# Optimization experiments

Measured on AMD Instinct MI355X. Metric: run time of the kernel, lower is better.

## Reference

```python
import jax, jax.numpy as jnp
import numpy as np

K = 1048576          # number of shooting particles (k); x also has K points
LR = 0.25            # fixed-point gradient-descent learning rate
N_ITERS = 20         # nr_of_fixed_point_iterations
nl = jnp.tanh        # nonlinearity='tanh'


def _advect(z, t1, b1, t2, b2):
    # z: [n, 2, 1]; t*: [2,2]; b*: [2,1]. dot z = theta1 @ nl(theta2 @ z + b2) + b1
    return jnp.matmul(t1, nl(jnp.matmul(t2, z) + b2)) + b1


def _lagrangian(t1, b1, t2, b2, q, p, invK, invKb):
    eye = jnp.eye(2, dtype=t1.dtype)
    v1 = t1.reshape(-1)
    v2 = (t2 - eye).reshape(-1)
    kinetic = 0.5 * (v1 @ invK @ v1 + v2 @ invK @ v2
                     + b1[:, 0] @ invKb @ b1[:, 0] + b2[:, 0] @ invKb @ b2[:, 0])
    potential = jnp.mean(p * _advect(q, t1, b1, t2, b2))
    return kinetic - potential


def _run_fixed_point(q, p, t1, b1, t2, b2, invK, invKb):
    grad_fn = jax.grad(_lagrangian, argnums=(0, 1, 2, 3))
    def step(carry, _):
        t1, b1, t2, b2 = carry
        g1, gb1, g2, gb2 = grad_fn(t1, b1, t2, b2, q, p, invK, invKb)
        return (t1 - LR * g1, b1 - LR * gb1, t2 - LR * g2, b2 - LR * gb2), None
    carry, _ = jax.lax.scan(step, (t1, b1, t2, b2), None, length=N_ITERS)
    return carry


def setup_inputs() -> dict:
    key = jax.random.key(0)
    k1, k2, k3, k4, k5 = jax.random.split(key, 5)
    inp = jax.random.normal(k1, (3 * K, 1, 2), dtype=jnp.float32)
    return {
        "t": jnp.zeros((1,), dtype=jnp.float32),
        "inp": inp,
        "theta1_init": jax.random.normal(k2, (2, 2), dtype=jnp.float32),
        "bias1_init": jax.random.normal(k3, (2, 1), dtype=jnp.float32),
        "theta2_init": jax.random.normal(k4, (2, 2), dtype=jnp.float32),
        "bias2_init": jax.random.normal(k5, (2, 1), dtype=jnp.float32),
        "inv_Kbar": jnp.eye(4, dtype=jnp.float32),    # Kbar = I(d^2) -> inverse = I
        "inv_Kbar_b": jnp.eye(2, dtype=jnp.float32),  # Kbar_b = I(d) -> inverse = I
        "k": K,
    }


def reference(t, inp, theta1_init, bias1_init, theta2_init, bias2_init,
              inv_Kbar, inv_Kbar_b, k):
    qt, pt, xt = inp[:k], inp[k:2 * k], inp[2 * k:]
    q = jnp.swapaxes(qt, 1, 2)  # [k, 2, 1]
    p = jnp.swapaxes(pt, 1, 2)
    x = jnp.swapaxes(xt, 1, 2)

    def final_thetas(qv):
        return _run_fixed_point(qv, p, theta1_init, bias1_init,
                                theta2_init, bias2_init, inv_Kbar, inv_Kbar_b)

    t1, b1, t2, b2 = final_thetas(q)

    # dot_p = dL/dq of the final Lagrangian, including dependence of the
    # fixed-point thetas on q (torch uses create_graph=True throughout).
    def L_of_q(qv):
        ft1, fb1, ft2, fb2 = final_thetas(qv)
        return _lagrangian(ft1, fb1, ft2, fb2, qv, p, inv_Kbar, inv_Kbar_b)

    dot_p = jax.grad(L_of_q)(q)
    dot_x = _advect(x, t1, b1, t2, b2)
    dot_q = _advect(q, t1, b1, t2, b2)

    return jnp.concatenate([jnp.swapaxes(dot_q, 1, 2),
                            jnp.swapaxes(dot_p, 1, 2),
                            jnp.swapaxes(dot_x, 1, 2)], axis=0)
```

## Files before the change

kernel.cpp:

```cpp
#include <hip/hip_runtime.h>


#define LR 0.25f
#define NIT 20
#define RTPB 512
#define NBR 256

typedef float v2f __attribute__((ext_vector_type(2)));

__device__ __forceinline__ v2f tanh2(v2f x){
    v2f e;
    e.x = __expf(x.x + x.x);
    e.y = __expf(x.y + x.y);
    v2f d = e + 1.0f;
    v2f r;
    r.x = __builtin_amdgcn_rcpf(d.x);
    r.y = __builtin_amdgcn_rcpf(d.y);
    return 1.0f - (r + r);
}

#define DPP_ADD(x, ctrl) ((x) + __int_as_float(__builtin_amdgcn_update_dpp(0, __float_as_int(x), (ctrl), 0xF, 0xF, true)))
__device__ __forceinline__ float wave_sum64(float x){
    x = DPP_ADD(x, 0x111);
    x = DPP_ADD(x, 0x112);
    x = DPP_ADD(x, 0x114);
    x = DPP_ADD(x, 0x118);
    x = DPP_ADD(x, 0x142);
    x = DPP_ADD(x, 0x143);
    return x;
}

__device__ __forceinline__ void compute_grad(const float* s, const float* th,
                                             const float* ksym, const float* ksymb,
                                             float c, float* g){
    const float Ivec[4]={1.f,0.f,0.f,1.f};
    #pragma unroll
    for(int j=0;j<4;j++){
        float kv=0.f;
        #pragma unroll
        for(int m=0;m<4;m++) kv += ksym[j*4+m]*th[m];
        g[j] = kv - c*s[j];
    }
    #pragma unroll
    for(int i2=0;i2<2;i2++)
        g[4+i2] = ksymb[i2*2+0]*th[4] + ksymb[i2*2+1]*th[5] - c*s[4+i2];
    #pragma unroll
    for(int j=0;j<4;j++){
        float kv=0.f;
        #pragma unroll
        for(int m=0;m<4;m++) kv += ksym[j*4+m]*(th[6+m]-Ivec[m]);
        g[6+j] = kv - c*s[6+j];
    }
    #pragma unroll
    for(int i2=0;i2<2;i2++)
        g[10+i2] = ksymb[i2*2+0]*th[10] + ksymb[i2*2+1]*th[11] - c*s[10+i2];
}

template<bool FULL>
__device__ __forceinline__ void accum_sample2(v2f Q0, v2f Q1, v2f P0, v2f P1,
    float t1_00,float t1_01,float t1_10,float t1_11,
    float t2_00,float t2_01,float t2_10,float t2_11,float b2_0,float b2_1,
    v2f* acc){
    v2f u0 = t2_00*Q0 + t2_01*Q1 + b2_0;
    v2f u1 = t2_10*Q0 + t2_11*Q1 + b2_1;
    v2f h0 = tanh2(u0), h1 = tanh2(u1);
    v2f s0 = 1.0f - h0*h0, s1 = 1.0f - h1*h1;
    v2f a0 = t1_00*P0 + t1_10*P1;
    v2f a1 = t1_01*P0 + t1_11*P1;
    v2f w0 = a0*s0, w1 = a1*s1;
    acc[0]+=P0*h0; acc[1]+=P0*h1; acc[2]+=P1*h0; acc[3]+=P1*h1;
    acc[4]+=P0;    acc[5]+=P1;
    acc[6]+=w0*Q0; acc[7]+=w0*Q1; acc[8]+=w1*Q0; acc[9]+=w1*Q1;
    acc[10]+=w0;   acc[11]+=w1;
    if(FULL){
        v2f r0 = -2.0f*(a0*h0)*s0, r1 = -2.0f*(a1*h1)*s1;
        v2f ps00=P0*s0, ps01=P0*s1, ps10=P1*s0, ps11=P1*s1;
        acc[12]+=ps00*Q0; acc[13]+=ps00*Q1; acc[14]+=ps01*Q0; acc[15]+=ps01*Q1;
        acc[16]+=ps10*Q0; acc[17]+=ps10*Q1; acc[18]+=ps11*Q0; acc[19]+=ps11*Q1;
        acc[20]+=ps00; acc[21]+=ps01; acc[22]+=ps10; acc[23]+=ps11;
        v2f r0q0=r0*Q0, r1q0=r1*Q0;
        acc[24]+=r0q0*Q0; acc[25]+=r0q0*Q1; acc[26]+=r0*(Q1*Q1);
        acc[27]+=r1q0*Q0; acc[28]+=r1q0*Q1; acc[29]+=r1*(Q1*Q1);
        acc[30]+=r0q0; acc[31]+=r0*Q1; acc[32]+=r1q0; acc[33]+=r1*Q1;
        acc[34]+=r0; acc[35]+=r1;
    }
}

template<bool FULL>
__global__ __launch_bounds__(RTPB) void k_reduce(
    const float4* __restrict__ q4, const float4* __restrict__ p4, int nv4,
    const float* __restrict__ t1i, const float* __restrict__ b1i,
    const float* __restrict__ t2i, const float* __restrict__ b2i,
    const float* __restrict__ invK, const float* __restrict__ invKb,
    const float* __restrict__ theta_prev,
    const float* __restrict__ part_prev,
    float* __restrict__ part_out,
    float* __restrict__ theta_out,
    float c)
{
    constexpr int NS = FULL ? 36 : 12;
    const int tid = threadIdx.x;
    const int NT = gridDim.x*RTPB;

    __shared__ float ths[12];
    __shared__ float sgv[12];
    __shared__ float tsum[12][33];
    __shared__ float red[RTPB/64][NS];
    __shared__ float ks[16], ksb[4];

    const bool structured = (nv4 == NBR*RTPB*4);
    float4 qd[4], pd[4];
    if(structured){
        const int xcd = blockIdx.x & 7, bi = blockIdx.x >> 3;
        const int sliceSz = nv4 >> 3;
        const int base = xcd*sliceSz + bi*RTPB + tid;
        #pragma unroll
        for(int s=0;s<4;s++){ qd[s]=q4[base + s*(32*RTPB)]; pd[s]=p4[base + s*(32*RTPB)]; }
    }

    if(!part_prev){
        if(tid < 12){
            float v = (tid<4)? t1i[tid] : (tid<6)? b1i[tid-4]
                    : (tid<10)? t2i[tid-6] : b2i[tid-10];
            ths[tid] = v;
            if(blockIdx.x==0) theta_out[tid] = v;
        }
        __syncthreads();
    }else{
        if(tid < 16) ks[tid]  = 0.5f*(invK[tid]  + invK[(tid&3)*4 + (tid>>2)]);
        if(tid < 4)  ksb[tid] = 0.5f*(invKb[tid] + invKb[(tid&1)*2 + (tid>>1)]);
        if(tid < 12*32){
            int j = tid >> 5, ch = tid & 31;
            const float* col = part_prev + j*NBR;
            float s = 0.f;
            #pragma unroll
            for(int i = 0; i < NBR/32; i++) s += col[ch + i*32];
            tsum[j][ch] = s;
        }
        __syncthreads();
        if(tid < 12){
            float s = 0.f;
            #pragma unroll
            for(int ch=0; ch<32; ch++) s += tsum[tid][ch];
            sgv[tid] = s;
        }
        __syncthreads();
        if(tid == 0){
            float g[12], tp[12];
            #pragma unroll
            for(int j=0;j<12;j++) tp[j] = theta_prev[j];
            compute_grad(sgv, tp, ks, ksb, c, g);
            #pragma unroll
            for(int j=0;j<12;j++){
                float t = tp[j] - LR*g[j];
                ths[j] = t;
                if(blockIdx.x==0) theta_out[j] = t;
            }
        }
        __syncthreads();
    }

    const float t1_00=ths[0], t1_01=ths[1], t1_10=ths[2], t1_11=ths[3];
    const float t2_00=ths[6], t2_01=ths[7], t2_10=ths[8], t2_11=ths[9];
    const float b2_0=ths[10], b2_1=ths[11];

    v2f acc[NS];
    #pragma unroll
    for(int j=0;j<NS;j++) acc[j] = (v2f){0.f, 0.f};

    if(structured){
        #pragma unroll
        for(int s=0;s<4;s++){
            v2f Q0={qd[s].x,qd[s].z}, Q1={qd[s].y,qd[s].w};
            v2f P0={pd[s].x,pd[s].z}, P1={pd[s].y,pd[s].w};
            accum_sample2<FULL>(Q0,Q1,P0,P1,
                t1_00,t1_01,t1_10,t1_11,t2_00,t2_01,t2_10,t2_11,b2_0,b2_1,acc);
        }
    }else{
        for(int j = blockIdx.x*RTPB + tid; j < nv4; j += NT){
            float4 qq = q4[j], pp = p4[j];
            v2f Q0={qq.x,qq.z}, Q1={qq.y,qq.w};
            v2f P0={pp.x,pp.z}, P1={pp.y,pp.w};
            accum_sample2<FULL>(Q0,Q1,P0,P1,
                t1_00,t1_01,t1_10,t1_11,t2_00,t2_01,t2_10,t2_11,b2_0,b2_1,acc);
        }
    }

    const int wave = tid >> 6;
    float wres[NS];
    #pragma unroll
    for(int j=0;j<NS;j++) wres[j] = wave_sum64(acc[j].x + acc[j].y);
    if((tid & 63) == 63){
        #pragma unroll
        for(int j=0;j<NS;j++) red[wave][j] = wres[j];
    }
    __syncthreads();
    if(tid < NS){
        float sum = 0.f;
        #pragma unroll
        for(int w=0; w<RTPB/64; w++) sum += red[w][tid];
        part_out[tid*NBR + blockIdx.x] = sum;
    }
}

__global__ __launch_bounds__(1024) void k_backfold(
    const float* __restrict__ part,
    const float* __restrict__ thetaAll,
    const float* __restrict__ invK, const float* __restrict__ invKb,
    float* __restrict__ pk_g, float c)
{
    const int tid = threadIdx.x;
    const int wave = tid >> 6, lane = tid & 63;
    __shared__ float sums[(NIT+1)*36];
    __shared__ float ks[16], ksb[4];
    if(tid < 16) ks[tid]  = 0.5f*(invK[tid]  + invK[(tid&3)*4 + (tid>>2)]);
    if(tid < 4)  ksb[tid] = 0.5f*(invKb[tid] + invKb[(tid&1)*2 + (tid>>1)]);

    for(int seg = wave; seg < (NIT+1)*36; seg += 16){
        int row = seg/36, col = seg - row*36;
        float s = 0.f;
        if(col < 12 || (row >= 1 && row <= 19)){
            const float* base = part + (size_t)seg*NBR;
            #pragma unroll
            for(int i = 0; i < NBR/64; i++) s += base[lane + i*64];
            s = wave_sum64(s);
        }
        if(lane == 63) sums[seg] = s;
    }
    __syncthreads();

    if(tid == 0){
        float lv[12];
        compute_grad(sums + 20*36, thetaAll + 20*12, ks, ksb, c, lv);
        for(int k=NIT-1;k>=0;k--){
            const float* s = sums + k*36;
            const float* T = thetaAll + k*12;
            float* P = pk_g + k*20;
            P[0]=T[0]; P[1]=T[1]; P[2]=T[2]; P[3]=T[3];
            P[4]=T[6]; P[5]=T[7]; P[6]=T[8]; P[7]=T[9];
            P[8]=T[10]; P[9]=T[11];
            P[10]=lv[0]; P[11]=lv[1]; P[12]=lv[2]; P[13]=lv[3];
            P[14]=lv[6]; P[15]=lv[7]; P[16]=lv[8]; P[17]=lv[9];
            P[18]=lv[10]; P[19]=lv[11];
            if(k==0) break;
            float H[12];
            for(int a=0;a<2;a++)for(int b=0;b<2;b++){
                int j=a*2+b;
                float data = s[12+a*4+b*2+0]*lv[6+b*2+0]
                           + s[12+a*4+b*2+1]*lv[6+b*2+1]
                           + s[20+a*2+b]*lv[10+b];
                float kv=0.f;
                for(int m=0;m<4;m++) kv += ks[j*4+m]*lv[m];
                H[j]=kv - c*data;
            }
            H[4] = ksb[0]*lv[4] + ksb[1]*lv[5];
            H[5] = ksb[2]*lv[4] + ksb[3]*lv[5];
            for(int cc=0;cc<2;cc++)for(int d=0;d<2;d++){
                int j=cc*2+d;
                float term1 = lv[0+cc]*s[12+0*4+cc*2+d] + lv[2+cc]*s[12+1*4+cc*2+d];
                float term2 = lv[6+cc*2+0]*s[24+cc*3+(0+d)] + lv[6+cc*2+1]*s[24+cc*3+(1+d)];
                float term3 = lv[10+cc]*s[30+cc*2+d];
                float kv=0.f;
                for(int m=0;m<4;m++) kv += ks[j*4+m]*lv[6+m];
                H[6+j]=kv - c*(term1+term2+term3);
            }
            for(int cc=0;cc<2;cc++){
                float z1 = lv[0+cc]*s[20+0*2+cc] + lv[2+cc]*s[20+1*2+cc];
                float z2 = lv[6+cc*2+0]*s[30+cc*2+0] + lv[6+cc*2+1]*s[30+cc*2+1];
                float z3 = lv[10+cc]*s[34+cc];
                float kv = ksb[cc*2+0]*lv[10] + ksb[cc*2+1]*lv[11];
                H[10+cc]=kv - c*(z1+z2+z3);
            }
            for(int j=0;j<12;j++) lv[j] -= LR*H[j];
        }
    }
}

__device__ __forceinline__ void bk_step2(v2f Q0, v2f Q1, v2f P0, v2f P1,
    float t1_00,float t1_01,float t1_10,float t1_11,
    float t2_00,float t2_01,float t2_10,float t2_11,float b2_0,float b2_1,
    float L1_00,float L1_01,float L1_10,float L1_11,
    float L2_00,float L2_01,float L2_10,float L2_11,float lb2_0,float lb2_1,
    v2f &B0, v2f &B1){
    v2f u0 = t2_00*Q0 + t2_01*Q1 + b2_0;
    v2f u1 = t2_10*Q0 + t2_11*Q1 + b2_1;
    v2f h0 = tanh2(u0), h1 = tanh2(u1);
    v2f s0 = 1.0f - h0*h0, s1 = 1.0f - h1*h1;
    v2f a0 = t1_00*P0 + t1_10*P1;
    v2f a1 = t1_01*P0 + t1_11*P1;
    v2f w0 = a0*s0, w1 = a1*s1;
    v2f r0 = -2.0f*(a0*h0)*s0, r1 = -2.0f*(a1*h1)*s1;
    v2f lp0 = L1_00*P0 + L1_10*P1;
    v2f lp1 = L1_01*P0 + L1_11*P1;
    v2f z0 = L2_00*Q0 + L2_01*Q1 + lb2_0;
    v2f z1 = L2_10*Q0 + L2_11*Q1 + lb2_1;
    v2f m0 = lp0*s0 + r0*z0;
    v2f m1 = lp1*s1 + r1*z1;
    B0 += t2_00*m0 + t2_10*m1 + L2_00*w0 + L2_10*w1;
    B1 += t2_01*m0 + t2_11*m1 + L2_01*w0 + L2_11*w1;
}

__global__ __launch_bounds__(256) void k_final(
    const float4* __restrict__ q4, const float4* __restrict__ p4,
    const float4* __restrict__ x4, int nv4,
    const float4* __restrict__ pk4, const float4* __restrict__ th20_4,
    float4* __restrict__ oq, float4* __restrict__ op, float4* __restrict__ ox,
    float c)
{
    __shared__ float4 pkS[NIT*5];
    __shared__ float4 t20[3];
    for(int j=threadIdx.x;j<NIT*5;j+=blockDim.x) pkS[j]=pk4[j];
    if(threadIdx.x<3) t20[threadIdx.x]=th20_4[threadIdx.x];
    __syncthreads();

    int j1, j2;
    const int fblk = gridDim.x;
    if((nv4 & 511) == 0 && (fblk & 7) == 0 && nv4 == fblk*512){
        const int xcd = blockIdx.x & 7, bi = blockIdx.x >> 3;
        j1 = xcd*(nv4>>3) + bi*512 + threadIdx.x;
        j2 = j1 + 256;
    }else{
        j1 = blockIdx.x*blockDim.x + threadIdx.x;
        j2 = j1 + fblk*256;
    }
    const bool v1 = (j1 < nv4), v2 = (j2 < nv4);

    v2f Q0a,Q1a,P0a,P1a, Q0b,Q1b,P0b,P1b;
    if(v1){ float4 qq=q4[j1], pp=p4[j1];
        Q0a=(v2f){qq.x,qq.z}; Q1a=(v2f){qq.y,qq.w};
        P0a=(v2f){pp.x,pp.z}; P1a=(v2f){pp.y,pp.w}; }
    if(v2){ float4 qq=q4[j2], pp=p4[j2];
        Q0b=(v2f){qq.x,qq.z}; Q1b=(v2f){qq.y,qq.w};
        P0b=(v2f){pp.x,pp.z}; P1b=(v2f){pp.y,pp.w}; }

    v2f B0a={0.f,0.f},B1a={0.f,0.f},B0b={0.f,0.f},B1b={0.f,0.f};
    #pragma unroll 4
    for(int k=0;k<NIT;k++){
        float4 P0=pkS[k*5+0], P1=pkS[k*5+1], P2=pkS[k*5+2], P3=pkS[k*5+3], P4v=pkS[k*5+4];
        float t1_00=P0.x,t1_01=P0.y,t1_10=P0.z,t1_11=P0.w;
        float t2_00=P1.x,t2_01=P1.y,t2_10=P1.z,t2_11=P1.w;
        float b2_0=P2.x,b2_1=P2.y;
        float L1_00=P2.z,L1_01=P2.w,L1_10=P3.x,L1_11=P3.y;
        float L2_00=P3.z,L2_01=P3.w,L2_10=P4v.x,L2_11=P4v.y,lb2_0=P4v.z,lb2_1=P4v.w;
        if(v1) bk_step2(Q0a,Q1a,P0a,P1a,
                t1_00,t1_01,t1_10,t1_11,t2_00,t2_01,t2_10,t2_11,b2_0,b2_1,
                L1_00,L1_01,L1_10,L1_11,L2_00,L2_01,L2_10,L2_11,lb2_0,lb2_1,B0a,B1a);
        if(v2) bk_step2(Q0b,Q1b,P0b,P1b,
                t1_00,t1_01,t1_10,t1_11,t2_00,t2_01,t2_10,t2_11,b2_0,b2_1,
                L1_00,L1_01,L1_10,L1_11,L2_00,L2_01,L2_10,L2_11,lb2_0,lb2_1,B0b,B1b);
    }

    float4 Ta=t20[0], Tb=t20[1], Tc=t20[2];
    float t1_00=Ta.x,t1_01=Ta.y,t1_10=Ta.z,t1_11=Ta.w,b1_0=Tb.x,b1_1=Tb.y;
    float t2_00=Tb.z,t2_01=Tb.w,t2_10=Tc.x,t2_11=Tc.y,b2_0=Tc.z,b2_1=Tc.w;

    #pragma unroll
    for(int sl=0; sl<2; sl++){
        bool v = sl? v2 : v1;
        if(!v) continue;
        int j = sl? j2 : j1;
        v2f Q0 = sl? Q0b:Q0a, Q1 = sl? Q1b:Q1a, P0 = sl? P0b:P0a, P1 = sl? P1b:P1a;
        v2f Bs0 = sl? B0b:B0a, Bs1 = sl? B1b:B1a;
        v2f u0 = t2_00*Q0 + t2_01*Q1 + b2_0;
        v2f u1 = t2_10*Q0 + t2_11*Q1 + b2_1;
        v2f h0 = tanh2(u0), h1 = tanh2(u1);
        v2f s0 = 1.0f - h0*h0, s1 = 1.0f - h1*h1;
        v2f a0 = t1_00*P0 + t1_10*P1;
        v2f a1 = t1_01*P0 + t1_11*P1;
        v2f w0 = a0*s0, w1 = a1*s1;
        v2f dq0 = t1_00*h0 + t1_01*h1 + b1_0;
        v2f dq1 = t1_10*h0 + t1_11*h1 + b1_1;
        v2f dp0 = c*(LR*Bs0 - (t2_00*w0 + t2_10*w1));
        v2f dp1 = c*(LR*Bs1 - (t2_01*w0 + t2_11*w1));
        oq[j] = make_float4(dq0.x, dq1.x, dq0.y, dq1.y);
        op[j] = make_float4(dp0.x, dp1.x, dp0.y, dp1.y);
        float4 xx = x4[j];
        v2f X0={xx.x,xx.z}, X1={xx.y,xx.w};
        v2f xu0 = t2_00*X0 + t2_01*X1 + b2_0;
        v2f xu1 = t2_10*X0 + t2_11*X1 + b2_1;
        v2f xh0 = tanh2(xu0), xh1 = tanh2(xu1);
        v2f xd0 = t1_00*xh0 + t1_01*xh1 + b1_0;
        v2f xd1 = t1_10*xh0 + t1_11*xh1 + b1_1;
        ox[j] = make_float4(xd0.x, xd1.x, xd0.y, xd1.y);
    }
}

extern "C" void kernel_launch(void* const* d_in, const int* in_sizes, int n_in,
                              void* d_out, int out_size, void* d_ws, size_t ws_size,
                              hipStream_t stream) {
    const float* inp = (const float*)d_in[1];
    const int K = in_sizes[1]/6;
    const int nv4 = K >> 1;

    const float4* q4 = (const float4*)inp;
    const float4* p4 = (const float4*)(inp + 2*(size_t)K);
    const float4* x4 = (const float4*)(inp + 4*(size_t)K);

    float* part  = (float*)d_ws;
    float* theta = part + (size_t)(NIT+1)*36*NBR;
    float* pk    = theta + 252;
    const float c = 1.0f/(2.0f*(float)K);

    const float* t1i = (const float*)d_in[2];
    const float* b1i = (const float*)d_in[3];
    const float* t2i = (const float*)d_in[4];
    const float* b2i = (const float*)d_in[5];
    const float* invK = (const float*)d_in[6];
    const float* invKb= (const float*)d_in[7];

    for(int k=0;k<=NIT;k++){
        const float* th_prev = (k==0) ? nullptr : theta + (k-1)*12;
        const float* pt_prev = (k==0) ? nullptr : part + (size_t)(k-1)*36*NBR;
        float* po = part + (size_t)k*36*NBR;
        float* to = theta + k*12;
        if(k==0 || k==NIT)
            k_reduce<false><<<NBR,RTPB,0,stream>>>(q4, p4, nv4,
                t1i, b1i, t2i, b2i, invK, invKb, th_prev, pt_prev, po, to, c);
        else
            k_reduce<true><<<NBR,RTPB,0,stream>>>(q4, p4, nv4,
                t1i, b1i, t2i, b2i, invK, invKb, th_prev, pt_prev, po, to, c);
    }
    k_backfold<<<1,1024,0,stream>>>(part, theta, invK, invKb, pk, c);

    float* out = (float*)d_out;
    int fthreads = (nv4 + 1)/2;
    int fblk = (fthreads + 255)/256;
    k_final<<<fblk,256,0,stream>>>(q4, p4, x4, nv4,
                                   (const float4*)pk, (const float4*)(theta + NIT*12),
                                   (float4*)out, (float4*)(out + 2*(size_t)K),
                                   (float4*)(out + 4*(size_t)K), c);
}
```

Baseline: 284.1 us.

## Fuse dot_q and dot_x outputs into last reduce pass; simplify final kernel

The last fixed-point reduce kernel (mode 2) now also computes and writes dot_q and dot_x. It reuses the q values it already holds in registers and loads x there, so the final kernel only computes dot_p. The final kernel drops its shared-memory staging and two-elements-per-thread scheme, reading the backfold parameters straight from global memory with one element per thread. The XCD-aware index mapping in the reduce kernel is replaced by a plain grid-stride layout, which may change L2 locality.

```diff
diff --git a/kernel.cpp b/kernel.cpp
--- a/kernel.cpp
+++ b/kernel.cpp
@@ -86,9 +86,10 @@
     }
 }
 
-template<bool FULL>
+template<int MODE>
 __global__ __launch_bounds__(RTPB) void k_reduce(
-    const float4* __restrict__ q4, const float4* __restrict__ p4, int nv4,
+    const float4* __restrict__ q4, const float4* __restrict__ p4,
+    const float4* __restrict__ x4, int nv4,
     const float* __restrict__ t1i, const float* __restrict__ b1i,
     const float* __restrict__ t2i, const float* __restrict__ b2i,
     const float* __restrict__ invK, const float* __restrict__ invKb,
@@ -96,11 +97,14 @@
     const float* __restrict__ part_prev,
     float* __restrict__ part_out,
     float* __restrict__ theta_out,
+    float4* __restrict__ oq, float4* __restrict__ ox,
     float c)
 {
+    constexpr bool FULL = (MODE==1);
     constexpr int NS = FULL ? 36 : 12;
     const int tid = threadIdx.x;
     const int NT = gridDim.x*RTPB;
+    const int gtid = blockIdx.x*RTPB + tid;
 
     __shared__ float ths[12];
     __shared__ float sgv[12];
@@ -111,14 +115,11 @@
     const bool structured = (nv4 == NBR*RTPB*4);
     float4 qd[4], pd[4];
     if(structured){
-        const int xcd = blockIdx.x & 7, bi = blockIdx.x >> 3;
-        const int sliceSz = nv4 >> 3;
-        const int base = xcd*sliceSz + bi*RTPB + tid;
-        #pragma unroll
-        for(int s=0;s<4;s++){ qd[s]=q4[base + s*(32*RTPB)]; pd[s]=p4[base + s*(32*RTPB)]; }
-    }
-
-    if(!part_prev){
+        #pragma unroll
+        for(int s=0;s<4;s++){ qd[s]=q4[gtid + s*NT]; pd[s]=p4[gtid + s*NT]; }
+    }
+
+    if(MODE==0){
         if(tid < 12){
             float v = (tid<4)? t1i[tid] : (tid<6)? b1i[tid-4]
                     : (tid<10)? t2i[tid-6] : b2i[tid-10];
@@ -177,7 +178,7 @@
                 t1_00,t1_01,t1_10,t1_11,t2_00,t2_01,t2_10,t2_11,b2_0,b2_1,acc);
         }
     }else{
-        for(int j = blockIdx.x*RTPB + tid; j < nv4; j += NT){
+        for(int j = gtid; j < nv4; j += NT){
             float4 qq = q4[j], pp = p4[j];
             v2f Q0={qq.x,qq.z}, Q1={qq.y,qq.w};
             v2f P0={pp.x,pp.z}, P1={pp.y,pp.w};
@@ -200,6 +201,51 @@
         #pragma unroll
         for(int w=0; w<RTPB/64; w++) sum += red[w][tid];
         part_out[tid*NBR + blockIdx.x] = sum;
+    }
+
+    if(MODE==2){
+        const float b1_0=ths[4], b1_1=ths[5];
+        if(structured){
+            float4 xd[4];
+            #pragma unroll
+            for(int s=0;s<4;s++) xd[s] = x4[gtid + s*NT];
+            #pragma unroll
+            for(int s=0;s<4;s++){
+                int j = gtid + s*NT;
+                v2f Q0={qd[s].x,qd[s].z}, Q1={qd[s].y,qd[s].w};
+                v2f u0 = t2_00*Q0 + t2_01*Q1 + b2_0;
+                v2f u1 = t2_10*Q0 + t2_11*Q1 + b2_1;
+                v2f h0 = tanh2(u0), h1 = tanh2(u1);
+                v2f dq0 = t1_00*h0 + t1_01*h1 + b1_0;
+                v2f dq1 = t1_10*h0 + t1_11*h1 + b1_1;
+                oq[j] = make_float4(dq0.x, dq1.x, dq0.y, dq1.y);
+                v2f X0={xd[s].x,xd[s].z}, X1={xd[s].y,xd[s].w};
+                v2f xu0 = t2_00*X0 + t2_01*X1 + b2_0;
+                v2f xu1 = t2_10*X0 + t2_11*X1 + b2_1;
+                v2f xh0 = tanh2(xu0), xh1 = tanh2(xu1);
+                v2f o0 = t1_00*xh0 + t1_01*xh1 + b1_0;
+                v2f o1 = t1_10*xh0 + t1_11*xh1 + b1_1;
+                ox[j] = make_float4(o0.x, o1.x, o0.y, o1.y);
+            }
+        }else{
+            for(int j = gtid; j < nv4; j += NT){
+                float4 qq = q4[j], xx = x4[j];
+                v2f Q0={qq.x,qq.z}, Q1={qq.y,qq.w};
+                v2f u0 = t2_00*Q0 + t2_01*Q1 + b2_0;
+                v2f u1 = t2_10*Q0 + t2_11*Q1 + b2_1;
+                v2f h0 = tanh2(u0), h1 = tanh2(u1);
+                v2f dq0 = t1_00*h0 + t1_01*h1 + b1_0;
+                v2f dq1 = t1_10*h0 + t1_11*h1 + b1_1;
+                oq[j] = make_float4(dq0.x, dq1.x, dq0.y, dq1.y);
+                v2f X0={xx.x,xx.z}, X1={xx.y,xx.w};
+                v2f xu0 = t2_00*X0 + t2_01*X1 + b2_0;
+                v2f xu1 = t2_10*X0 + t2_11*X1 + b2_1;
+                v2f xh0 = tanh2(xu0), xh1 = tanh2(xu1);
+                v2f o0 = t1_00*xh0 + t1_01*xh1 + b1_0;
+                v2f o1 = t1_10*xh0 + t1_11*xh1 + b1_1;
+                ox[j] = make_float4(o0.x, o1.x, o0.y, o1.y);
+            }
+        }
     }
 }
 
@@ -301,88 +347,39 @@
 }
 
 __global__ __launch_bounds__(256) void k_final(
-    const float4* __restrict__ q4, const float4* __restrict__ p4,
-    const float4* __restrict__ x4, int nv4,
-    const float4* __restrict__ pk4, const float4* __restrict__ th20_4,
-    float4* __restrict__ oq, float4* __restrict__ op, float4* __restrict__ ox,
-    float c)
+    const float4* __restrict__ q4, const float4* __restrict__ p4, int nv4,
+    const float4* __restrict__ pk4,
+    const float4* __restrict__ th20_4,
+    float4* __restrict__ op, float c)
 {
-    __shared__ float4 pkS[NIT*5];
-    __shared__ float4 t20[3];
-    for(int j=threadIdx.x;j<NIT*5;j+=blockDim.x) pkS[j]=pk4[j];
-    if(threadIdx.x<3) t20[threadIdx.x]=th20_4[threadIdx.x];
-    __syncthreads();
-
-    int j1, j2;
-    const int fblk = gridDim.x;
-    if((nv4 & 511) == 0 && (fblk & 7) == 0 && nv4 == fblk*512){
-        const int xcd = blockIdx.x & 7, bi = blockIdx.x >> 3;
-        j1 = xcd*(nv4>>3) + bi*512 + threadIdx.x;
-        j2 = j1 + 256;
-    }else{
-        j1 = blockIdx.x*blockDim.x + threadIdx.x;
-        j2 = j1 + fblk*256;
-    }
-    const bool v1 = (j1 < nv4), v2 = (j2 < nv4);
-
-    v2f Q0a,Q1a,P0a,P1a, Q0b,Q1b,P0b,P1b;
-    if(v1){ float4 qq=q4[j1], pp=p4[j1];
-        Q0a=(v2f){qq.x,qq.z}; Q1a=(v2f){qq.y,qq.w};
-        P0a=(v2f){pp.x,pp.z}; P1a=(v2f){pp.y,pp.w}; }
-    if(v2){ float4 qq=q4[j2], pp=p4[j2];
-        Q0b=(v2f){qq.x,qq.z}; Q1b=(v2f){qq.y,qq.w};
-        P0b=(v2f){pp.x,pp.z}; P1b=(v2f){pp.y,pp.w}; }
-
-    v2f B0a={0.f,0.f},B1a={0.f,0.f},B0b={0.f,0.f},B1b={0.f,0.f};
-    #pragma unroll 4
+    const int j = blockIdx.x*blockDim.x + threadIdx.x;
+    if(j >= nv4) return;
+    float4 qq=q4[j], pp=p4[j];
+    v2f Q0={qq.x,qq.z}, Q1={qq.y,qq.w}, P0={pp.x,pp.z}, P1={pp.y,pp.w};
+    v2f B0={0.f,0.f}, B1={0.f,0.f};
+    #pragma unroll 5
     for(int k=0;k<NIT;k++){
-        float4 P0=pkS[k*5+0], P1=pkS[k*5+1], P2=pkS[k*5+2], P3=pkS[k*5+3], P4v=pkS[k*5+4];
-        float t1_00=P0.x,t1_01=P0.y,t1_10=P0.z,t1_11=P0.w;
-        float t2_00=P1.x,t2_01=P1.y,t2_10=P1.z,t2_11=P1.w;
-        float b2_0=P2.x,b2_1=P2.y;
-        float L1_00=P2.z,L1_01=P2.w,L1_10=P3.x,L1_11=P3.y;
-        float L2_00=P3.z,L2_01=P3.w,L2_10=P4v.x,L2_11=P4v.y,lb2_0=P4v.z,lb2_1=P4v.w;
-        if(v1) bk_step2(Q0a,Q1a,P0a,P1a,
-                t1_00,t1_01,t1_10,t1_11,t2_00,t2_01,t2_10,t2_11,b2_0,b2_1,
-                L1_00,L1_01,L1_10,L1_11,L2_00,L2_01,L2_10,L2_11,lb2_0,lb2_1,B0a,B1a);
-        if(v2) bk_step2(Q0b,Q1b,P0b,P1b,
-                t1_00,t1_01,t1_10,t1_11,t2_00,t2_01,t2_10,t2_11,b2_0,b2_1,
-                L1_00,L1_01,L1_10,L1_11,L2_00,L2_01,L2_10,L2_11,lb2_0,lb2_1,B0b,B1b);
-    }
-
-    float4 Ta=t20[0], Tb=t20[1], Tc=t20[2];
-    float t1_00=Ta.x,t1_01=Ta.y,t1_10=Ta.z,t1_11=Ta.w,b1_0=Tb.x,b1_1=Tb.y;
-    float t2_00=Tb.z,t2_01=Tb.w,t2_10=Tc.x,t2_11=Tc.y,b2_0=Tc.z,b2_1=Tc.w;
-
-    #pragma unroll
-    for(int sl=0; sl<2; sl++){
-        bool v = sl? v2 : v1;
-        if(!v) continue;
-        int j = sl? j2 : j1;
-        v2f Q0 = sl? Q0b:Q0a, Q1 = sl? Q1b:Q1a, P0 = sl? P0b:P0a, P1 = sl? P1b:P1a;
-        v2f Bs0 = sl? B0b:B0a, Bs1 = sl? B1b:B1a;
-        v2f u0 = t2_00*Q0 + t2_01*Q1 + b2_0;
-        v2f u1 = t2_10*Q0 + t2_11*Q1 + b2_1;
-        v2f h0 = tanh2(u0), h1 = tanh2(u1);
-        v2f s0 = 1.0f - h0*h0, s1 = 1.0f - h1*h1;
-        v2f a0 = t1_00*P0 + t1_10*P1;
-        v2f a1 = t1_01*P0 + t1_11*P1;
-        v2f w0 = a0*s0, w1 = a1*s1;
-        v2f dq0 = t1_00*h0 + t1_01*h1 + b1_0;
-        v2f dq1 = t1_10*h0 + t1_11*h1 + b1_1;
-        v2f dp0 = c*(LR*Bs0 - (t2_00*w0 + t2_10*w1));
-        v2f dp1 = c*(LR*Bs1 - (t2_01*w0 + t2_11*w1));
-        oq[j] = make_float4(dq0.x, dq1.x, dq0.y, dq1.y);
-        op[j] = make_float4(dp0.x, dp1.x, dp0.y, dp1.y);
-        float4 xx = x4[j];
-        v2f X0={xx.x,xx.z}, X1={xx.y,xx.w};
-        v2f xu0 = t2_00*X0 + t2_01*X1 + b2_0;
-        v2f xu1 = t2_10*X0 + t2_11*X1 + b2_1;
-        v2f xh0 = tanh2(xu0), xh1 = tanh2(xu1);
-        v2f xd0 = t1_00*xh0 + t1_01*xh1 + b1_0;
-        v2f xd1 = t1_10*xh0 + t1_11*xh1 + b1_1;
-        ox[j] = make_float4(xd0.x, xd1.x, xd0.y, xd1.y);
-    }
+        float4 Pa=pk4[k*5+0], Pb=pk4[k*5+1], Pc=pk4[k*5+2], Pd=pk4[k*5+3], Pe=pk4[k*5+4];
+        bk_step2(Q0,Q1,P0,P1,
+                 Pa.x,Pa.y,Pa.z,Pa.w,
+                 Pb.x,Pb.y,Pb.z,Pb.w,
+                 Pc.x,Pc.y,
+                 Pc.z,Pc.w,Pd.x,Pd.y,
+                 Pd.z,Pd.w,Pe.x,Pe.y,
+                 Pe.z,Pe.w,
+                 B0,B1);
+    }
+    float4 Ta=th20_4[0], Tb=th20_4[1], Tc=th20_4[2];
+    v2f u0 = Tb.z*Q0 + Tb.w*Q1 + Tc.z;
+    v2f u1 = Tc.x*Q0 + Tc.y*Q1 + Tc.w;
+    v2f h0 = tanh2(u0), h1 = tanh2(u1);
+    v2f s0 = 1.0f - h0*h0, s1 = 1.0f - h1*h1;
+    v2f a0 = Ta.x*P0 + Ta.z*P1;
+    v2f a1 = Ta.y*P0 + Ta.w*P1;
+    v2f w0 = a0*s0, w1 = a1*s1;
+    v2f dp0 = c*(LR*B0 - (Tb.z*w0 + Tc.x*w1));
+    v2f dp1 = c*(LR*B1 - (Tb.w*w0 + Tc.y*w1));
+    op[j] = make_float4(dp0.x, dp1.x, dp0.y, dp1.y);
 }
 
 extern "C" void kernel_launch(void* const* d_in, const int* in_sizes, int n_in,
@@ -408,25 +405,30 @@
     const float* invK = (const float*)d_in[6];
     const float* invKb= (const float*)d_in[7];
 
+    float* out = (float*)d_out;
+    float4* oq = (float4*)out;
+    float4* op = (float4*)(out + 2*(size_t)K);
+    float4* ox = (float4*)(out + 4*(size_t)K);
+
     for(int k=0;k<=NIT;k++){
         const float* th_prev = (k==0) ? nullptr : theta + (k-1)*12;
         const float* pt_prev = (k==0) ? nullptr : part + (size_t)(k-1)*36*NBR;
         float* po = part + (size_t)k*36*NBR;
         float* to = theta + k*12;
-        if(k==0 || k==NIT)
-            k_reduce<false><<<NBR,RTPB,0,stream>>>(q4, p4, nv4,
-                t1i, b1i, t2i, b2i, invK, invKb, th_prev, pt_prev, po, to, c);
+        if(k==0)
+            k_reduce<0><<<NBR,RTPB,0,stream>>>(q4, p4, x4, nv4,
+                t1i, b1i, t2i, b2i, invK, invKb, th_prev, pt_prev, po, to, oq, ox, c);
+        else if(k==NIT)
+            k_reduce<2><<<NBR,RTPB,0,stream>>>(q4, p4, x4, nv4,
+                t1i, b1i, t2i, b2i, invK, invKb, th_prev, pt_prev, po, to, oq, ox, c);
         else
-            k_reduce<true><<<NBR,RTPB,0,stream>>>(q4, p4, nv4,
-                t1i, b1i, t2i, b2i, invK, invKb, th_prev, pt_prev, po, to, c);
+            k_reduce<1><<<NBR,RTPB,0,stream>>>(q4, p4, x4, nv4,
+                t1i, b1i, t2i, b2i, invK, invKb, th_prev, pt_prev, po, to, oq, ox, c);
     }
     k_backfold<<<1,1024,0,stream>>>(part, theta, invK, invKb, pk, c);
 
-    float* out = (float*)d_out;
-    int fthreads = (nv4 + 1)/2;
-    int fblk = (fthreads + 255)/256;
-    k_final<<<fblk,256,0,stream>>>(q4, p4, x4, nv4,
+    int fblk = (nv4 + 255)/256;
+    k_final<<<fblk,256,0,stream>>>(q4, p4, nv4,
                                    (const float4*)pk, (const float4*)(theta + NIT*12),
-                                   (float4*)out, (float4*)(out + 2*(size_t)K),
-                                   (float4*)(out + 4*(size_t)K), c);
-}
+                                   op, c);
+}
```

New measurement: 282.7 us. About the same (-0.5%).
